# Kernel tuning notes

Measured on AMD Instinct MI355X. Metric: run time of the kernel, lower is better.

## Reference

```python
import jax, jax.numpy as jnp
import numpy as np

N_NODES = 100000
N_EDGES = 1250000
D_FEAT = 64


def setup_inputs() -> dict:
    key = jax.random.key(0)
    kx, ke = jax.random.split(key)
    x = jax.random.normal(kx, (N_NODES, D_FEAT), dtype=jnp.float32)
    edge_index = jax.random.randint(ke, (2, N_EDGES), 0, N_NODES, dtype=jnp.int64)
    return {"x": x, "edge_index": edge_index}


def reference(x, edge_index):
    # propagate: scatter_nested gathers x[idxj] grouped by destination idxi
    # (a ragged per-node neighbor set); the module's sum_nested reduces each
    # group. Expressed densely and jit-ably as gather + segment-sum.
    idxi = edge_index[0, :]  # destination nodes
    idxj = edge_index[1, :]  # source nodes
    messages = x[idxj]  # [E, D] edge-level gather (memory-bound)
    out = jax.ops.segment_sum(messages, idxi, num_segments=N_NODES)  # [N, D]
    return out
```

## Files before the change

kernel.cpp:

```cpp
#include <hip/hip_runtime.h>

#define N_NODES 100000
#define N_EDGES 1250000
#define D_FEAT  64

#define NPB     392
#define NBINS   256
#define BCAP    6144
#define HALF    196
#define HCAP    3328
#define K23B    (NBINS * 2)
#define EPB     5120
#define EPT     10
#define K1B     ((N_EDGES + EPB - 1) / EPB)
#define OVF_CAP 32768

__global__ __launch_bounds__(512) void k1_bin_kernel(
        const int* __restrict__ idxi, const int* __restrict__ idxj,
        int* __restrict__ gcursor, int* __restrict__ ovfcnt,
        int* __restrict__ ovf, int* __restrict__ binbuf) {
    __shared__ int hist[NBINS];
    __shared__ int runstart[NBINS];
    __shared__ int gbase[NBINS];
    __shared__ int cur[NBINS];
    __shared__ int staged[EPB];
    __shared__ unsigned char sbin[EPB];
    int t = threadIdx.x;
    if (t < NBINS) hist[t] = 0;
    __syncthreads();

    int base = blockIdx.x * EPB;
    int n = N_EDGES - base; if (n > EPB) n = EPB;

    int d[EPT], s[EPT], bn[EPT];
#pragma unroll
    for (int j = 0; j < EPT; ++j) {
        int i = t + j * 512;
        if (i < n) { d[j] = idxi[base + i]; s[j] = idxj[base + i]; }
        else       { d[j] = -1; s[j] = 0; }
    }
#pragma unroll
    for (int j = 0; j < EPT; ++j) {
        bn[j] = (d[j] >= 0) ? (d[j] / NPB) : -1;
        if (bn[j] >= 0) atomicAdd(&hist[bn[j]], 1);
    }
    __syncthreads();

    if (t < 64) {
        int b0 = t * 4;
        int h0 = hist[b0], h1 = hist[b0 + 1], h2 = hist[b0 + 2], h3 = hist[b0 + 3];
        int s01 = h0 + h1;
        int sum = s01 + h2 + h3;
        int inc = sum;
#pragma unroll
        for (int off = 1; off < 64; off <<= 1) {
            int u = __shfl_up(inc, off, 64);
            if (t >= off) inc += u;
        }
        int ex = inc - sum;
        runstart[b0]     = ex;
        runstart[b0 + 1] = ex + h0;
        runstart[b0 + 2] = ex + s01;
        runstart[b0 + 3] = ex + s01 + h2;
    }
    __syncthreads();

    if (t < NBINS) {
        int h = hist[t];
        gbase[t] = h ? atomicAdd(&gcursor[t], h) : 0;
        cur[t] = 0;
    }
    __syncthreads();

#pragma unroll
    for (int j = 0; j < EPT; ++j) {
        if (bn[j] >= 0) {
            int idx = runstart[bn[j]] + atomicAdd(&cur[bn[j]], 1);
            staged[idx] = ((d[j] - bn[j] * NPB) << 17) | s[j];
            sbin[idx] = (unsigned char)bn[j];
        }
    }
    __syncthreads();

    for (int i = t; i < n; i += 512) {
        int b = sbin[i];
        int p = staged[i];
        int tgt = gbase[b] + (i - runstart[b]);
        if (tgt < BCAP) {
            binbuf[b * BCAP + tgt] = p;
        } else {
            int op = atomicAdd(ovfcnt, 1);
            if (op < OVF_CAP) { ovf[2 * op] = b * NPB + (p >> 17); ovf[2 * op + 1] = p & 0x1FFFF; }
        }
    }
}

__global__ __launch_bounds__(1024, 8) void k23_fused_kernel(
        const float* __restrict__ x, const int* __restrict__ gcursor,
        const int* __restrict__ binbuf, const int* __restrict__ ovfcnt,
        const int* __restrict__ ovf, float* __restrict__ out) {
    __shared__ int cnt[HALF];
    __shared__ int excl[HALF];
    __shared__ int cur[HALF];
    __shared__ int srt[HCAP];
    int blk = blockIdx.x;
    int bin = blk >> 1;
    int hi  = blk & 1;
    int lobase = hi * HALF;
    int t = threadIdx.x;
    if (t < HALF) cnt[t] = 0;
    __syncthreads();

    int n = gcursor[bin];
    if (n > BCAP) n = BCAP;
    const int* src = binbuf + (size_t)bin * BCAP;

    int p[6];
#pragma unroll
    for (int j = 0; j < 6; ++j) {
        int i = t + j * 1024;
        p[j] = (i < n) ? src[i] : -1;
    }
#pragma unroll
    for (int j = 0; j < 6; ++j) {
        if (p[j] >= 0) {
            int loc = (p[j] >> 17) - lobase;
            if ((unsigned)loc < HALF) atomicAdd(&cnt[loc], 1);
            else p[j] = -1;
        }
    }
    __syncthreads();

    if (t < 64) {
        int h[4];
        int sum = 0;
#pragma unroll
        for (int q = 0; q < 4; ++q) {
            int b = t * 4 + q;
            h[q] = (b < HALF) ? cnt[b] : 0;
            sum += h[q];
        }
        int inc = sum;
#pragma unroll
        for (int off = 1; off < 64; off <<= 1) {
            int u = __shfl_up(inc, off, 64);
            if (t >= off) inc += u;
        }
        int ex = inc - sum;
#pragma unroll
        for (int q = 0; q < 4; ++q) {
            int b = t * 4 + q;
            if (b < HALF) { excl[b] = ex; cur[b] = 0; }
            ex += h[q];
        }
    }
    __syncthreads();

#pragma unroll
    for (int j = 0; j < 6; ++j) {
        if (p[j] >= 0) {
            int loc = (p[j] >> 17) - lobase;
            int pos = excl[loc] + atomicAdd(&cur[loc], 1);
            if (pos < HCAP) srt[pos] = p[j] & 0x1FFFF;
        }
    }
    __syncthreads();

    int sg = t >> 4, c4 = t & 15;
    const float4* xp = (const float4*)x;
#pragma unroll
    for (int i2 = 0; i2 < 4; ++i2) {
        int dl = sg + (i2 << 6);
        if (dl >= HALF) break;
        int node = bin * NPB + lobase + dl;
        int k = excl[dl];
        int end = k + cnt[dl];
        if (end > HCAP) end = HCAP;
        float4 acc = make_float4(0.f, 0.f, 0.f, 0.f);
        for (; k + 8 <= end; k += 8) {
            int a0 = srt[k],     a1 = srt[k + 1], a2 = srt[k + 2], a3 = srt[k + 3];
            int a4 = srt[k + 4], a5 = srt[k + 5], a6 = srt[k + 6], a7 = srt[k + 7];
            float4 v0 = xp[a0 * 16 + c4];
            float4 v1 = xp[a1 * 16 + c4];
            float4 v2 = xp[a2 * 16 + c4];
            float4 v3 = xp[a3 * 16 + c4];
            float4 v4 = xp[a4 * 16 + c4];
            float4 v5 = xp[a5 * 16 + c4];
            float4 v6 = xp[a6 * 16 + c4];
            float4 v7 = xp[a7 * 16 + c4];
            acc.x += ((v0.x + v1.x) + (v2.x + v3.x)) + ((v4.x + v5.x) + (v6.x + v7.x));
            acc.y += ((v0.y + v1.y) + (v2.y + v3.y)) + ((v4.y + v5.y) + (v6.y + v7.y));
            acc.z += ((v0.z + v1.z) + (v2.z + v3.z)) + ((v4.z + v5.z) + (v6.z + v7.z));
            acc.w += ((v0.w + v1.w) + (v2.w + v3.w)) + ((v4.w + v5.w) + (v6.w + v7.w));
        }
        if (k + 4 <= end) {
            int a0 = srt[k], a1 = srt[k + 1], a2 = srt[k + 2], a3 = srt[k + 3];
            float4 v0 = xp[a0 * 16 + c4];
            float4 v1 = xp[a1 * 16 + c4];
            float4 v2 = xp[a2 * 16 + c4];
            float4 v3 = xp[a3 * 16 + c4];
            acc.x += (v0.x + v1.x) + (v2.x + v3.x);
            acc.y += (v0.y + v1.y) + (v2.y + v3.y);
            acc.z += (v0.z + v1.z) + (v2.z + v3.z);
            acc.w += (v0.w + v1.w) + (v2.w + v3.w);
            k += 4;
        }
        for (; k < end; ++k) {
            float4 v0 = xp[srt[k] * 16 + c4];
            acc.x += v0.x; acc.y += v0.y; acc.z += v0.z; acc.w += v0.w;
        }
        if (node < N_NODES)
            ((float4*)out)[(size_t)node * 16 + c4] = acc;
    }

    __syncthreads();
    int novf = *ovfcnt;
    if (novf > 0) {
        __threadfence();
        if (novf > OVF_CAP) novf = OVF_CAP;
        int lo = bin * NPB + lobase;
        for (int e = t; e < novf; e += 1024) {
            int dnode = ovf[2 * e];
            if ((unsigned)(dnode - lo) < HALF && dnode < N_NODES) {
                int snode = ovf[2 * e + 1];
                const float* vsrc = x + (size_t)snode * D_FEAT;
                float* o = out + (size_t)dnode * D_FEAT;
                for (int f = 0; f < D_FEAT; ++f) atomicAdd(o + f, vsrc[f]);
            }
        }
    }
}


__global__ __launch_bounds__(256) void zero_f4_kernel(float* __restrict__ out, int n4) {
    int i = blockIdx.x * blockDim.x + threadIdx.x;
    if (i < n4) ((float4*)out)[i] = make_float4(0.f, 0.f, 0.f, 0.f);
}

__global__ __launch_bounds__(256) void scatter_add_kernel(const float* __restrict__ x,
                                                          const int* __restrict__ idxi,
                                                          const int* __restrict__ idxj,
                                                          float* __restrict__ out) {
    int t = blockIdx.x * blockDim.x + threadIdx.x;
    int e = t >> 4;
    if (e >= N_EDGES) return;
    int fo = (t & 15) << 2;
    int dst = idxi[e];
    int src = idxj[e];
    const float4 v = *(const float4*)(x + (size_t)src * D_FEAT + fo);
    float* o = out + (size_t)dst * D_FEAT + fo;
    atomicAdd(o + 0, v.x);
    atomicAdd(o + 1, v.y);
    atomicAdd(o + 2, v.z);
    atomicAdd(o + 3, v.w);
}

extern "C" void kernel_launch(void* const* d_in, const int* in_sizes, int n_in,
                              void* d_out, int out_size, void* d_ws, size_t ws_size,
                              hipStream_t stream) {
    const float* x  = (const float*)d_in[0];
    const int*   ei = (const int*)d_in[1];
    const int*   idxi = ei;
    const int*   idxj = ei + N_EDGES;
    float* out = (float*)d_out;

    {
        size_t need = (256 + 16 + 2 * (size_t)OVF_CAP +
                       (size_t)NBINS * BCAP) * sizeof(int);
        if (ws_size >= need) {
            int* gcursor = (int*)d_ws;
            int* ovfcnt  = gcursor + 256;
            int* ovf     = ovfcnt + 16;
            int* binbuf  = ovf + 2 * OVF_CAP;

            hipMemsetAsync(gcursor, 0, (256 + 16) * sizeof(int), stream);
            k1_bin_kernel<<<K1B, 512, 0, stream>>>(idxi, idxj, gcursor, ovfcnt, ovf, binbuf);
            k23_fused_kernel<<<K23B, 1024, 0, stream>>>(x, gcursor, binbuf, ovfcnt, ovf, out);
            return;
        }
    }

    int n4 = (N_NODES * D_FEAT) / 4;
    zero_f4_kernel<<<(n4 + 255) / 256, 256, 0, stream>>>(out, n4);
    long long total_threads = (long long)N_EDGES * 16;
    scatter_add_kernel<<<(int)((total_threads + 255) / 256), 256, 0, stream>>>(x, idxi, idxj, out);
}
```

Measured before the change: 132.6 us.

## Replace atomic bin-cursor reservation with histogram, scan, and deterministic scatter passes

The binning stage is split into three kernels. A per-block histogram pass runs first, then a per-bin exclusive scan across blocks, then a scatter pass that writes to precomputed offsets, so global atomics on bin cursors and the memset are no longer needed. Blocks are also smaller (256 threads, 1280 edges each), which raises the block count and shrinks shared staging per block. In exchange, idxi is read twice and there are two extra launches plus an intermediate histogram buffer. The old single-pass path stays as a fallback for small workspaces.

```diff
diff --git a/kernel.cpp b/kernel.cpp
--- a/kernel.cpp
+++ b/kernel.cpp
@@ -10,14 +10,69 @@
 #define HALF    196
 #define HCAP    3328
 #define K23B    (NBINS * 2)
-#define EPB     5120
-#define EPT     10
-#define K1B     ((N_EDGES + EPB - 1) / EPB)
 #define OVF_CAP 32768
 
-__global__ __launch_bounds__(512) void k1_bin_kernel(
+#define K1T     256
+#define EPB     1280
+#define EPT     5
+#define NB1     ((N_EDGES + EPB - 1) / EPB)
+#define CHUNK   16
+
+#define L_EPB   5120
+#define L_EPT   10
+#define L_K1B   ((N_EDGES + L_EPB - 1) / L_EPB)
+
+__global__ __launch_bounds__(K1T) void k1a_hist_kernel(
+        const int* __restrict__ idxi, int* __restrict__ H) {
+    __shared__ int hist[NBINS];
+    int t = threadIdx.x;
+    if (t < NBINS) hist[t] = 0;
+    __syncthreads();
+
+    int base = blockIdx.x * EPB;
+    int n = N_EDGES - base; if (n > EPB) n = EPB;
+#pragma unroll
+    for (int j = 0; j < EPT; ++j) {
+        int i = t + j * K1T;
+        if (i < n) atomicAdd(&hist[idxi[base + i] / NPB], 1);
+    }
+    __syncthreads();
+    if (t < NBINS) H[blockIdx.x * NBINS + t] = hist[t];
+}
+
+__global__ __launch_bounds__(64) void k1s_scan_kernel(
+        const int* __restrict__ H, int* __restrict__ B,
+        int* __restrict__ gcursor, int* __restrict__ ovfcnt) {
+    int bin = blockIdx.x;
+    int l = threadIdx.x;
+    int h[CHUNK];
+    int sum = 0;
+#pragma unroll
+    for (int q = 0; q < CHUNK; ++q) {
+        int blk = l * CHUNK + q;
+        h[q] = (blk < NB1) ? H[blk * NBINS + bin] : 0;
+        sum += h[q];
+    }
+    int inc = sum;
+#pragma unroll
+    for (int off = 1; off < 64; off <<= 1) {
+        int u = __shfl_up(inc, off, 64);
+        if (l >= off) inc += u;
+    }
+    int ex = inc - sum;
+#pragma unroll
+    for (int q = 0; q < CHUNK; ++q) {
+        int blk = l * CHUNK + q;
+        if (blk < NB1) B[blk * NBINS + bin] = ex;
+        ex += h[q];
+    }
+    if (l == 63) gcursor[bin] = inc;
+    if (bin == 0 && l == 0) *ovfcnt = 0;
+}
+
+__global__ __launch_bounds__(K1T) void k1b_scatter_kernel(
         const int* __restrict__ idxi, const int* __restrict__ idxj,
-        int* __restrict__ gcursor, int* __restrict__ ovfcnt,
+        const int* __restrict__ B, int* __restrict__ ovfcnt,
         int* __restrict__ ovf, int* __restrict__ binbuf) {
     __shared__ int hist[NBINS];
     __shared__ int runstart[NBINS];
@@ -35,7 +90,7 @@
     int d[EPT], s[EPT], bn[EPT];
 #pragma unroll
     for (int j = 0; j < EPT; ++j) {
-        int i = t + j * 512;
+        int i = t + j * K1T;
         if (i < n) { d[j] = idxi[base + i]; s[j] = idxj[base + i]; }
         else       { d[j] = -1; s[j] = 0; }
     }
@@ -66,6 +121,85 @@
     __syncthreads();
 
     if (t < NBINS) {
+        gbase[t] = B[blockIdx.x * NBINS + t];
+        cur[t] = 0;
+    }
+    __syncthreads();
+
+#pragma unroll
+    for (int j = 0; j < EPT; ++j) {
+        if (bn[j] >= 0) {
+            int idx = runstart[bn[j]] + atomicAdd(&cur[bn[j]], 1);
+            staged[idx] = ((d[j] - bn[j] * NPB) << 17) | s[j];
+            sbin[idx] = (unsigned char)bn[j];
+        }
+    }
+    __syncthreads();
+
+    for (int i = t; i < n; i += K1T) {
+        int b = sbin[i];
+        int p = staged[i];
+        int tgt = gbase[b] + (i - runstart[b]);
+        if (tgt < BCAP) {
+            binbuf[b * BCAP + tgt] = p;
+        } else {
+            int op = atomicAdd(ovfcnt, 1);
+            if (op < OVF_CAP) { ovf[2 * op] = b * NPB + (p >> 17); ovf[2 * op + 1] = p & 0x1FFFF; }
+        }
+    }
+}
+
+__global__ __launch_bounds__(512) void k1_bin_kernel(
+        const int* __restrict__ idxi, const int* __restrict__ idxj,
+        int* __restrict__ gcursor, int* __restrict__ ovfcnt,
+        int* __restrict__ ovf, int* __restrict__ binbuf) {
+    __shared__ int hist[NBINS];
+    __shared__ int runstart[NBINS];
+    __shared__ int gbase[NBINS];
+    __shared__ int cur[NBINS];
+    __shared__ int staged[L_EPB];
+    __shared__ unsigned char sbin[L_EPB];
+    int t = threadIdx.x;
+    if (t < NBINS) hist[t] = 0;
+    __syncthreads();
+
+    int base = blockIdx.x * L_EPB;
+    int n = N_EDGES - base; if (n > L_EPB) n = L_EPB;
+
+    int d[L_EPT], s[L_EPT], bn[L_EPT];
+#pragma unroll
+    for (int j = 0; j < L_EPT; ++j) {
+        int i = t + j * 512;
+        if (i < n) { d[j] = idxi[base + i]; s[j] = idxj[base + i]; }
+        else       { d[j] = -1; s[j] = 0; }
+    }
+#pragma unroll
+    for (int j = 0; j < L_EPT; ++j) {
+        bn[j] = (d[j] >= 0) ? (d[j] / NPB) : -1;
+        if (bn[j] >= 0) atomicAdd(&hist[bn[j]], 1);
+    }
+    __syncthreads();
+
+    if (t < 64) {
+        int b0 = t * 4;
+        int h0 = hist[b0], h1 = hist[b0 + 1], h2 = hist[b0 + 2], h3 = hist[b0 + 3];
+        int s01 = h0 + h1;
+        int sum = s01 + h2 + h3;
+        int inc = sum;
+#pragma unroll
+        for (int off = 1; off < 64; off <<= 1) {
+            int u = __shfl_up(inc, off, 64);
+            if (t >= off) inc += u;
+        }
+        int ex = inc - sum;
+        runstart[b0]     = ex;
+        runstart[b0 + 1] = ex + h0;
+        runstart[b0 + 2] = ex + s01;
+        runstart[b0 + 3] = ex + s01 + h2;
+    }
+    __syncthreads();
+
+    if (t < NBINS) {
         int h = hist[t];
         gbase[t] = h ? atomicAdd(&gcursor[t], h) : 0;
         cur[t] = 0;
@@ -73,7 +207,7 @@
     __syncthreads();
 
 #pragma unroll
-    for (int j = 0; j < EPT; ++j) {
+    for (int j = 0; j < L_EPT; ++j) {
         if (bn[j] >= 0) {
             int idx = runstart[bn[j]] + atomicAdd(&cur[bn[j]], 1);
             staged[idx] = ((d[j] - bn[j] * NPB) << 17) | s[j];
@@ -266,6 +400,26 @@
 
     {
         size_t need = (256 + 16 + 2 * (size_t)OVF_CAP +
+                       2 * (size_t)NB1 * NBINS +
+                       (size_t)NBINS * BCAP) * sizeof(int);
+        if (ws_size >= need) {
+            int* gcursor = (int*)d_ws;
+            int* ovfcnt  = gcursor + 256;
+            int* ovf     = ovfcnt + 16;
+            int* H       = ovf + 2 * OVF_CAP;
+            int* B       = H + (size_t)NB1 * NBINS;
+            int* binbuf  = B + (size_t)NB1 * NBINS;
+
+            k1a_hist_kernel<<<NB1, K1T, 0, stream>>>(idxi, H);
+            k1s_scan_kernel<<<NBINS, 64, 0, stream>>>(H, B, gcursor, ovfcnt);
+            k1b_scatter_kernel<<<NB1, K1T, 0, stream>>>(idxi, idxj, B, ovfcnt, ovf, binbuf);
+            k23_fused_kernel<<<K23B, 1024, 0, stream>>>(x, gcursor, binbuf, ovfcnt, ovf, out);
+            return;
+        }
+    }
+
+    {
+        size_t need = (256 + 16 + 2 * (size_t)OVF_CAP +
                        (size_t)NBINS * BCAP) * sizeof(int);
         if (ws_size >= need) {
             int* gcursor = (int*)d_ws;
@@ -274,7 +428,7 @@
             int* binbuf  = ovf + 2 * OVF_CAP;
 
             hipMemsetAsync(gcursor, 0, (256 + 16) * sizeof(int), stream);
-            k1_bin_kernel<<<K1B, 512, 0, stream>>>(idxi, idxj, gcursor, ovfcnt, ovf, binbuf);
+            k1_bin_kernel<<<L_K1B, 512, 0, stream>>>(idxi, idxj, gcursor, ovfcnt, ovf, binbuf);
             k23_fused_kernel<<<K23B, 1024, 0, stream>>>(x, gcursor, binbuf, ovfcnt, ovf, out);
             return;
         }
```

New measurement: 135.6 us. +2.2%, slower.

## Gather fp16 copy of features, converting x inside binning kernel

Applied to the files above, without the earlier changes.

Adds extra blocks to the binning kernel that convert x to half precision into workspace. The gather/reduce kernel then reads 16-byte fp16 chunks, eight threads per node, and accumulates in fp32. This roughly halves gather traffic at the cost of a conversion pass and reduced input precision. Edges per block in the binning kernel are also halved.

```diff
diff --git a/kernel.cpp b/kernel.cpp
--- a/kernel.cpp
+++ b/kernel.cpp
@@ -1,4 +1,5 @@
 #include <hip/hip_runtime.h>
+#include <hip/hip_fp16.h>
 
 #define N_NODES 100000
 #define N_EDGES 1250000
@@ -10,21 +11,37 @@
 #define HALF    196
 #define HCAP    3328
 #define K23B    (NBINS * 2)
-#define EPB     5120
-#define EPT     10
+#define EPB     2560
+#define EPT     5
 #define K1B     ((N_EDGES + EPB - 1) / EPB)
+#define CONVB   246
 #define OVF_CAP 32768
-
-__global__ __launch_bounds__(512) void k1_bin_kernel(
+#define XH_INTS (N_NODES * (D_FEAT / 2))
+
+__global__ __launch_bounds__(512) void k1_bin_conv_kernel(
         const int* __restrict__ idxi, const int* __restrict__ idxj,
         int* __restrict__ gcursor, int* __restrict__ ovfcnt,
-        int* __restrict__ ovf, int* __restrict__ binbuf) {
+        int* __restrict__ ovf, int* __restrict__ binbuf,
+        const float* __restrict__ x, unsigned int* __restrict__ xh) {
     __shared__ int hist[NBINS];
     __shared__ int runstart[NBINS];
     __shared__ int gbase[NBINS];
     __shared__ int cur[NBINS];
     __shared__ int staged[EPB];
     __shared__ unsigned char sbin[EPB];
+
+    if (blockIdx.x >= K1B) {
+        int t0 = (blockIdx.x - K1B) * 512 + threadIdx.x;
+        int stride = CONVB * 512;
+        const float2* x2 = (const float2*)x;
+        for (int i = t0; i < XH_INTS; i += stride) {
+            float2 v = x2[i];
+            __half2 h = __floats2half2_rn(v.x, v.y);
+            xh[i] = *(unsigned int*)&h;
+        }
+        return;
+    }
+
     int t = threadIdx.x;
     if (t < NBINS) hist[t] = 0;
     __syncthreads();
@@ -95,18 +112,29 @@
     }
 }
 
-__global__ __launch_bounds__(1024, 8) void k23_fused_kernel(
-        const float* __restrict__ x, const int* __restrict__ gcursor,
-        const int* __restrict__ binbuf, const int* __restrict__ ovfcnt,
-        const int* __restrict__ ovf, float* __restrict__ out) {
+__device__ __forceinline__ void cvt8(uint4 u, float4& a, float4& b) {
+    __half2 h0 = *reinterpret_cast<__half2*>(&u.x);
+    __half2 h1 = *reinterpret_cast<__half2*>(&u.y);
+    __half2 h2 = *reinterpret_cast<__half2*>(&u.z);
+    __half2 h3 = *reinterpret_cast<__half2*>(&u.w);
+    float2 f0 = __half22float2(h0), f1 = __half22float2(h1);
+    float2 f2 = __half22float2(h2), f3 = __half22float2(h3);
+    a = make_float4(f0.x, f0.y, f1.x, f1.y);
+    b = make_float4(f2.x, f2.y, f3.x, f3.y);
+}
+
+__global__ __launch_bounds__(1024, 8) void k23_fp16_kernel(
+        const float* __restrict__ x, const unsigned int* __restrict__ xh,
+        const int* __restrict__ gcursor, const int* __restrict__ binbuf,
+        const int* __restrict__ ovfcnt, const int* __restrict__ ovf,
+        float* __restrict__ out) {
     __shared__ int cnt[HALF];
     __shared__ int excl[HALF];
     __shared__ int cur[HALF];
     __shared__ int srt[HCAP];
     int blk = blockIdx.x;
     int bin = blk >> 1;
-    int hi  = blk & 1;
-    int lobase = hi * HALF;
+    int lobase = (blk & 1) * HALF;
     int t = threadIdx.x;
     if (t < HALF) cnt[t] = 0;
     __syncthreads();
@@ -166,51 +194,42 @@
     }
     __syncthreads();
 
-    int sg = t >> 4, c4 = t & 15;
-    const float4* xp = (const float4*)x;
-#pragma unroll
-    for (int i2 = 0; i2 < 4; ++i2) {
-        int dl = sg + (i2 << 6);
-        if (dl >= HALF) break;
+    int sg = t >> 3, c8 = t & 7;
+    const uint4* xp = (const uint4*)xh;
+    for (int dl = sg; dl < HALF; dl += 128) {
         int node = bin * NPB + lobase + dl;
         int k = excl[dl];
         int end = k + cnt[dl];
         if (end > HCAP) end = HCAP;
-        float4 acc = make_float4(0.f, 0.f, 0.f, 0.f);
-        for (; k + 8 <= end; k += 8) {
-            int a0 = srt[k],     a1 = srt[k + 1], a2 = srt[k + 2], a3 = srt[k + 3];
-            int a4 = srt[k + 4], a5 = srt[k + 5], a6 = srt[k + 6], a7 = srt[k + 7];
-            float4 v0 = xp[a0 * 16 + c4];
-            float4 v1 = xp[a1 * 16 + c4];
-            float4 v2 = xp[a2 * 16 + c4];
-            float4 v3 = xp[a3 * 16 + c4];
-            float4 v4 = xp[a4 * 16 + c4];
-            float4 v5 = xp[a5 * 16 + c4];
-            float4 v6 = xp[a6 * 16 + c4];
-            float4 v7 = xp[a7 * 16 + c4];
-            acc.x += ((v0.x + v1.x) + (v2.x + v3.x)) + ((v4.x + v5.x) + (v6.x + v7.x));
-            acc.y += ((v0.y + v1.y) + (v2.y + v3.y)) + ((v4.y + v5.y) + (v6.y + v7.y));
-            acc.z += ((v0.z + v1.z) + (v2.z + v3.z)) + ((v4.z + v5.z) + (v6.z + v7.z));
-            acc.w += ((v0.w + v1.w) + (v2.w + v3.w)) + ((v4.w + v5.w) + (v6.w + v7.w));
-        }
-        if (k + 4 <= end) {
-            int a0 = srt[k], a1 = srt[k + 1], a2 = srt[k + 2], a3 = srt[k + 3];
-            float4 v0 = xp[a0 * 16 + c4];
-            float4 v1 = xp[a1 * 16 + c4];
-            float4 v2 = xp[a2 * 16 + c4];
-            float4 v3 = xp[a3 * 16 + c4];
-            acc.x += (v0.x + v1.x) + (v2.x + v3.x);
-            acc.y += (v0.y + v1.y) + (v2.y + v3.y);
-            acc.z += (v0.z + v1.z) + (v2.z + v3.z);
-            acc.w += (v0.w + v1.w) + (v2.w + v3.w);
-            k += 4;
+        float4 accA = make_float4(0.f, 0.f, 0.f, 0.f);
+        float4 accB = make_float4(0.f, 0.f, 0.f, 0.f);
+        for (; k + 4 <= end; k += 4) {
+            uint4 u0 = xp[(size_t)srt[k]     * 8 + c8];
+            uint4 u1 = xp[(size_t)srt[k + 1] * 8 + c8];
+            uint4 u2 = xp[(size_t)srt[k + 2] * 8 + c8];
+            uint4 u3 = xp[(size_t)srt[k + 3] * 8 + c8];
+            float4 a0, b0, a1, b1, a2, b2, a3, b3;
+            cvt8(u0, a0, b0); cvt8(u1, a1, b1); cvt8(u2, a2, b2); cvt8(u3, a3, b3);
+            accA.x += (a0.x + a1.x) + (a2.x + a3.x);
+            accA.y += (a0.y + a1.y) + (a2.y + a3.y);
+            accA.z += (a0.z + a1.z) + (a2.z + a3.z);
+            accA.w += (a0.w + a1.w) + (a2.w + a3.w);
+            accB.x += (b0.x + b1.x) + (b2.x + b3.x);
+            accB.y += (b0.y + b1.y) + (b2.y + b3.y);
+            accB.z += (b0.z + b1.z) + (b2.z + b3.z);
+            accB.w += (b0.w + b1.w) + (b2.w + b3.w);
         }
         for (; k < end; ++k) {
-            float4 v0 = xp[srt[k] * 16 + c4];
-            acc.x += v0.x; acc.y += v0.y; acc.z += v0.z; acc.w += v0.w;
-        }
-        if (node < N_NODES)
-            ((float4*)out)[(size_t)node * 16 + c4] = acc;
+            uint4 u0 = xp[(size_t)srt[k] * 8 + c8];
+            float4 a0, b0;
+            cvt8(u0, a0, b0);
+            accA.x += a0.x; accA.y += a0.y; accA.z += a0.z; accA.w += a0.w;
+            accB.x += b0.x; accB.y += b0.y; accB.z += b0.z; accB.w += b0.w;
+        }
+        if (node < N_NODES) {
+            ((float4*)out)[(size_t)node * 16 + (c8 << 1)]     = accA;
+            ((float4*)out)[(size_t)node * 16 + (c8 << 1) + 1] = accB;
+        }
     }
 
     __syncthreads();
@@ -265,17 +284,20 @@
     float* out = (float*)d_out;
 
     {
-        size_t need = (256 + 16 + 2 * (size_t)OVF_CAP +
+        size_t need = (256 + 16 + 2 * (size_t)OVF_CAP + (size_t)XH_INTS +
                        (size_t)NBINS * BCAP) * sizeof(int);
         if (ws_size >= need) {
             int* gcursor = (int*)d_ws;
             int* ovfcnt  = gcursor + 256;
             int* ovf     = ovfcnt + 16;
-            int* binbuf  = ovf + 2 * OVF_CAP;
+            unsigned int* xh = (unsigned int*)(ovf + 2 * OVF_CAP);
+            int* binbuf  = (int*)(xh + XH_INTS);
 
             hipMemsetAsync(gcursor, 0, (256 + 16) * sizeof(int), stream);
-            k1_bin_kernel<<<K1B, 512, 0, stream>>>(idxi, idxj, gcursor, ovfcnt, ovf, binbuf);
-            k23_fused_kernel<<<K23B, 1024, 0, stream>>>(x, gcursor, binbuf, ovfcnt, ovf, out);
+            k1_bin_conv_kernel<<<K1B + CONVB, 512, 0, stream>>>(
+                idxi, idxj, gcursor, ovfcnt, ovf, binbuf, x, xh);
+            k23_fp16_kernel<<<K23B, 1024, 0, stream>>>(x, xh, gcursor, binbuf,
+                                                       ovfcnt, ovf, out);
             return;
         }
     }
```

Result: slower. 135.6 us (+2.3%).
